# Optimization experiments

Measured on AMD Instinct MI355X. Metric: run time of the kernel, lower is better.

The kernel has to match this reference:

```python
import jax, jax.numpy as jnp
import numpy as np

N_NODES = 10000
IN_CH = 128
OUT_CH = 128
N_EDGES = 320000


def setup_inputs() -> dict:
    key = jax.random.key(0)
    k1, k2, k3, k4 = jax.random.split(key, 4)
    x = jax.random.normal(k1, (N_NODES, IN_CH), dtype=jnp.float32)
    edge_index = jax.random.randint(k2, (N_EDGES, 2), 0, N_NODES, dtype=jnp.int64)
    # Linear weights (torch stores [out, in]); scale like kaiming-uniform-ish
    w = jax.random.normal(k3, (OUT_CH, IN_CH), dtype=jnp.float32) / np.sqrt(IN_CH)
    b = jax.random.normal(k4, (OUT_CH, IN_CH), dtype=jnp.float32) / np.sqrt(IN_CH)
    return {"x": x, "edge_index": edge_index, "w": w, "b": b}


def reference(x, edge_index, w, b):
    n = x.shape[0]
    # Each edge (i, j) contributes x[j] to node i and x[i] to node j (undirected).
    src = jnp.concatenate([edge_index[:, 1], edge_index[:, 0]])  # feature source
    dst = jnp.concatenate([edge_index[:, 0], edge_index[:, 1]])  # aggregation target
    # segment-sum of gathered neighbor features -> [n, in_ch]
    agg_sum = jax.ops.segment_sum(x[src], dst, num_segments=n)
    deg = jax.ops.segment_sum(jnp.ones_like(dst, dtype=x.dtype), dst, num_segments=n)
    # mean with zero fallback for isolated nodes (original uses zeros vector)
    agg = jnp.where(deg[:, None] > 0, agg_sum / jnp.maximum(deg, 1.0)[:, None], 0.0)
    # out = ReLU(agg @ w^T + x @ b^T)
    return jax.nn.relu(agg @ w.T + x @ b.T)
```

## Files before the change

### kernel.cpp

```cpp
#include <hip/hip_runtime.h>

#define N_NODES 10000
#define CH 128
#define N_EDGES 320000
#define CAP 128
#define CSTR 16


__device__ __forceinline__ unsigned short f2bf(float f) {
    unsigned u = __float_as_uint(f);
    return (unsigned short)((u + 0x7FFFu + ((u >> 16) & 1u)) >> 16);
}
__device__ __forceinline__ float bf2f(unsigned short h) {
    return __uint_as_float(((unsigned)h) << 16);
}

__global__ __launch_bounds__(256) void fill_kernel(const int* __restrict__ ei,
                                                   int* __restrict__ cursor,
                                                   unsigned short* __restrict__ adj)
{
    const int t = blockIdx.x * blockDim.x + threadIdx.x;
    if (t >= N_EDGES) return;
    const int2 p = ((const int2*)ei)[t];
    if ((unsigned)p.x >= N_NODES || (unsigned)p.y >= N_NODES) return;
    const int s0 = atomicAdd(&cursor[p.x * CSTR], 1);
    const int s1 = atomicAdd(&cursor[p.y * CSTR], 1);
    if (s0 < CAP) adj[(size_t)p.x * CAP + s0] = (unsigned short)p.y;
    if (s1 < CAP) adj[(size_t)p.y * CAP + s1] = (unsigned short)p.x;
}

__global__ __launch_bounds__(256) void gather_kernel(const float* __restrict__ x,
                                                     const int* __restrict__ cursor,
                                                     const unsigned short* __restrict__ adj,
                                                     unsigned short* __restrict__ aggb)
{
    const int wv   = threadIdx.x >> 6;
    const int node = blockIdx.x * 4 + wv;
    const int lane = threadIdx.x & 63;
    const int h    = lane >> 5;
    const int l    = lane & 31;

    const int deg = cursor[node * CSTR];
    const int d   = deg < CAP ? deg : CAP;
    const unsigned short* nb = adj + (size_t)node * CAP;

    float4 acc = {0.f, 0.f, 0.f, 0.f};
    const int nit = (d + 1) >> 1;
#pragma unroll 4
    for (int it = 0; it < nit; ++it) {
        const int idx = 2 * it + h;
        int j = nb[idx];
        j = j < N_NODES ? j : 0;
        const float4 u = ((const float4*)(x + (size_t)j * CH))[l];
        const float m = idx < d ? 1.0f : 0.0f;
        acc.x += m * u.x; acc.y += m * u.y; acc.z += m * u.z; acc.w += m * u.w;
    }
    acc.x += __shfl_xor(acc.x, 32, 64);
    acc.y += __shfl_xor(acc.y, 32, 64);
    acc.z += __shfl_xor(acc.z, 32, 64);
    acc.w += __shfl_xor(acc.w, 32, 64);

    if (h == 0) {
        const float inv = deg > 0 ? 1.0f / (float)deg : 0.0f;
        ushort4 o;
        o.x = f2bf(acc.x * inv);
        o.y = f2bf(acc.y * inv);
        o.z = f2bf(acc.z * inv);
        o.w = f2bf(acc.w * inv);
        ((ushort4*)(aggb + (size_t)node * CH))[l] = o;
    }
}

#define NPB 16
__global__ __launch_bounds__(256) void gemm_relu_kernel(const unsigned short* __restrict__ aggb,
                                                        const float* __restrict__ x,
                                                        const float* __restrict__ w,
                                                        const float* __restrict__ b,
                                                        float* __restrict__ out)
{
    __shared__ float sh_a[NPB * CH];
    __shared__ float sh_x[NPB * CH];
    const int tid   = threadIdx.x;
    const int node0 = blockIdx.x * NPB;

    const ushort4* ag = (const ushort4*)(aggb + (size_t)node0 * CH);
#pragma unroll
    for (int r = 0; r < 2; ++r) {
        const ushort4 q = ag[tid + r * 256];
        const int base = (tid + r * 256) * 4;
        sh_a[base + 0] = bf2f(q.x);
        sh_a[base + 1] = bf2f(q.y);
        sh_a[base + 2] = bf2f(q.z);
        sh_a[base + 3] = bf2f(q.w);
    }
    ((float4*)sh_x)[tid]       = ((const float4*)(x + (size_t)node0 * CH))[tid];
    ((float4*)sh_x)[tid + 256] = ((const float4*)(x + (size_t)node0 * CH))[tid + 256];
    __syncthreads();

    const int o = tid & 127;
    const int g = tid >> 7;
    const float4* wr = (const float4*)(w + (size_t)o * CH);
    const float4* br = (const float4*)(b + (size_t)o * CH);
    const float4* A  = (const float4*)(sh_a + (size_t)(g * 8) * CH);
    const float4* X  = (const float4*)(sh_x + (size_t)(g * 8) * CH);

    float acc[8] = {0.f, 0.f, 0.f, 0.f, 0.f, 0.f, 0.f, 0.f};
#pragma unroll 4
    for (int k = 0; k < CH / 4; ++k) {
        const float4 wv = wr[k];
        const float4 bv = br[k];
#pragma unroll
        for (int n = 0; n < 8; ++n) {
            const float4 a4 = A[n * (CH / 4) + k];
            const float4 x4 = X[n * (CH / 4) + k];
            acc[n] += a4.x * wv.x + a4.y * wv.y + a4.z * wv.z + a4.w * wv.w
                    + x4.x * bv.x + x4.y * bv.y + x4.z * bv.z + x4.w * bv.w;
        }
    }
#pragma unroll
    for (int n = 0; n < 8; ++n) {
        const int node = node0 + g * 8 + n;
        const float v = acc[n];
        out[(size_t)node * CH + o] = v > 0.f ? v : 0.f;
    }
}

extern "C" void kernel_launch(void* const* d_in, const int* in_sizes, int n_in,
                              void* d_out, int out_size, void* d_ws, size_t ws_size,
                              hipStream_t stream)
{
    const float* x  = (const float*)d_in[0];
    const int*   ei = (const int*)d_in[1];
    const float* w  = (const float*)d_in[2];
    const float* b  = (const float*)d_in[3];
    float*       out = (float*)d_out;

    int*            cursor = (int*)d_ws;
    unsigned short* adj    = (unsigned short*)((char*)d_ws + 640000);
    unsigned short* aggb   = (unsigned short*)((char*)d_ws + 3200000);

    hipMemsetAsync(d_ws, 0, (size_t)N_NODES * CSTR * sizeof(int), stream);

    fill_kernel<<<(N_EDGES + 255) / 256, 256, 0, stream>>>(ei, cursor, adj);
    gather_kernel<<<N_NODES / 4, 256, 0, stream>>>(x, cursor, adj, aggb);
    gemm_relu_kernel<<<N_NODES / NPB, 256, 0, stream>>>(aggb, x, w, b, out);
}
```

Measured before the change: 140.4 us.

## Fuse gather into GEMM and gather from a bf16 copy of x

Adds a bf16 conversion of x to the edge-fill kernel, with each thread now handling two edges and converting eight floats. The gather is folded into the GEMM kernel: each block aggregates its 16 nodes straight into shared memory, so the aggregated intermediate is never written to or read back from global memory. Neighbour rows are read as bf16, halving gather traffic. The cost is fewer gather blocks (625 instead of 2500), which cuts the parallelism available to hide the random-access latency, and it adds bf16 rounding to the neighbour features.

```diff
diff --git a/kernel.cpp b/kernel.cpp
--- a/kernel.cpp
+++ b/kernel.cpp
@@ -5,6 +5,7 @@
 #define N_EDGES 320000
 #define CAP 128
 #define CSTR 16
+#define NPB 16
 
 
 __device__ __forceinline__ unsigned short f2bf(float f) {
@@ -15,86 +16,96 @@
     return __uint_as_float(((unsigned)h) << 16);
 }
 
-__global__ __launch_bounds__(256) void fill_kernel(const int* __restrict__ ei,
-                                                   int* __restrict__ cursor,
-                                                   unsigned short* __restrict__ adj)
+__global__ __launch_bounds__(256) void fill_convert_kernel(
+    const int* __restrict__ ei,
+    const float* __restrict__ x,
+    int* __restrict__ cursor,
+    unsigned short* __restrict__ adj,
+    unsigned short* __restrict__ xb)
 {
     const int t = blockIdx.x * blockDim.x + threadIdx.x;
-    if (t >= N_EDGES) return;
-    const int2 p = ((const int2*)ei)[t];
-    if ((unsigned)p.x >= N_NODES || (unsigned)p.y >= N_NODES) return;
-    const int s0 = atomicAdd(&cursor[p.x * CSTR], 1);
-    const int s1 = atomicAdd(&cursor[p.y * CSTR], 1);
-    if (s0 < CAP) adj[(size_t)p.x * CAP + s0] = (unsigned short)p.y;
-    if (s1 < CAP) adj[(size_t)p.y * CAP + s1] = (unsigned short)p.x;
-}
 
-__global__ __launch_bounds__(256) void gather_kernel(const float* __restrict__ x,
-                                                     const int* __restrict__ cursor,
-                                                     const unsigned short* __restrict__ adj,
-                                                     unsigned short* __restrict__ aggb)
-{
-    const int wv   = threadIdx.x >> 6;
-    const int node = blockIdx.x * 4 + wv;
-    const int lane = threadIdx.x & 63;
-    const int h    = lane >> 5;
-    const int l    = lane & 31;
+    const float4 c0 = ((const float4*)x)[2 * t];
+    const float4 c1 = ((const float4*)x)[2 * t + 1];
+    ushort4 o0, o1;
+    o0.x = f2bf(c0.x); o0.y = f2bf(c0.y); o0.z = f2bf(c0.z); o0.w = f2bf(c0.w);
+    o1.x = f2bf(c1.x); o1.y = f2bf(c1.y); o1.z = f2bf(c1.z); o1.w = f2bf(c1.w);
+    ((ushort4*)xb)[2 * t]     = o0;
+    ((ushort4*)xb)[2 * t + 1] = o1;
 
-    const int deg = cursor[node * CSTR];
-    const int d   = deg < CAP ? deg : CAP;
-    const unsigned short* nb = adj + (size_t)node * CAP;
-
-    float4 acc = {0.f, 0.f, 0.f, 0.f};
-    const int nit = (d + 1) >> 1;
-#pragma unroll 4
-    for (int it = 0; it < nit; ++it) {
-        const int idx = 2 * it + h;
-        int j = nb[idx];
-        j = j < N_NODES ? j : 0;
-        const float4 u = ((const float4*)(x + (size_t)j * CH))[l];
-        const float m = idx < d ? 1.0f : 0.0f;
-        acc.x += m * u.x; acc.y += m * u.y; acc.z += m * u.z; acc.w += m * u.w;
+    const int4 p = ((const int4*)ei)[t];
+    const bool v0 = (unsigned)p.x < N_NODES && (unsigned)p.y < N_NODES;
+    const bool v1 = (unsigned)p.z < N_NODES && (unsigned)p.w < N_NODES;
+    int s0 = 0, s1 = 0, s2 = 0, s3 = 0;
+    if (v0) { s0 = atomicAdd(&cursor[p.x * CSTR], 1); s1 = atomicAdd(&cursor[p.y * CSTR], 1); }
+    if (v1) { s2 = atomicAdd(&cursor[p.z * CSTR], 1); s3 = atomicAdd(&cursor[p.w * CSTR], 1); }
+    if (v0) {
+        if (s0 < CAP) adj[(size_t)p.x * CAP + s0] = (unsigned short)p.y;
+        if (s1 < CAP) adj[(size_t)p.y * CAP + s1] = (unsigned short)p.x;
     }
-    acc.x += __shfl_xor(acc.x, 32, 64);
-    acc.y += __shfl_xor(acc.y, 32, 64);
-    acc.z += __shfl_xor(acc.z, 32, 64);
-    acc.w += __shfl_xor(acc.w, 32, 64);
-
-    if (h == 0) {
-        const float inv = deg > 0 ? 1.0f / (float)deg : 0.0f;
-        ushort4 o;
-        o.x = f2bf(acc.x * inv);
-        o.y = f2bf(acc.y * inv);
-        o.z = f2bf(acc.z * inv);
-        o.w = f2bf(acc.w * inv);
-        ((ushort4*)(aggb + (size_t)node * CH))[l] = o;
+    if (v1) {
+        if (s2 < CAP) adj[(size_t)p.z * CAP + s2] = (unsigned short)p.w;
+        if (s3 < CAP) adj[(size_t)p.w * CAP + s3] = (unsigned short)p.z;
     }
 }
 
-#define NPB 16
-__global__ __launch_bounds__(256) void gemm_relu_kernel(const unsigned short* __restrict__ aggb,
-                                                        const float* __restrict__ x,
-                                                        const float* __restrict__ w,
-                                                        const float* __restrict__ b,
-                                                        float* __restrict__ out)
+__global__ __launch_bounds__(256) void gather_gemm_kernel(
+    const float* __restrict__ x,
+    const unsigned short* __restrict__ xb,
+    const int* __restrict__ cursor,
+    const unsigned short* __restrict__ adj,
+    const float* __restrict__ w,
+    const float* __restrict__ b,
+    float* __restrict__ out)
 {
     __shared__ float sh_a[NPB * CH];
     __shared__ float sh_x[NPB * CH];
     const int tid   = threadIdx.x;
     const int node0 = blockIdx.x * NPB;
 
-    const ushort4* ag = (const ushort4*)(aggb + (size_t)node0 * CH);
-#pragma unroll
-    for (int r = 0; r < 2; ++r) {
-        const ushort4 q = ag[tid + r * 256];
-        const int base = (tid + r * 256) * 4;
-        sh_a[base + 0] = bf2f(q.x);
-        sh_a[base + 1] = bf2f(q.y);
-        sh_a[base + 2] = bf2f(q.z);
-        sh_a[base + 3] = bf2f(q.w);
-    }
     ((float4*)sh_x)[tid]       = ((const float4*)(x + (size_t)node0 * CH))[tid];
     ((float4*)sh_x)[tid + 256] = ((const float4*)(x + (size_t)node0 * CH))[tid + 256];
+
+    {
+        const int wv   = tid >> 6;
+        const int lane = tid & 63;
+        const int h    = lane >> 5;
+        const int l    = lane & 31;
+#pragma unroll
+        for (int q = 0; q < 4; ++q) {
+            const int ln   = wv + 4 * q;
+            const int node = node0 + ln;
+            const int deg  = cursor[node * CSTR];
+            const int d    = deg < CAP ? deg : CAP;
+            const unsigned short* nb = adj + (size_t)node * CAP;
+
+            float4 acc = {0.f, 0.f, 0.f, 0.f};
+            const int nit = (d + 1) >> 1;
+#pragma unroll 4
+            for (int it = 0; it < nit; ++it) {
+                const int idx = 2 * it + h;
+                int j = nb[idx];
+                j = j < N_NODES ? j : 0;
+                const ushort4 u = ((const ushort4*)(xb + (size_t)j * CH))[l];
+                const float m = idx < d ? 1.0f : 0.0f;
+                acc.x += m * bf2f(u.x);
+                acc.y += m * bf2f(u.y);
+                acc.z += m * bf2f(u.z);
+                acc.w += m * bf2f(u.w);
+            }
+            acc.x += __shfl_xor(acc.x, 32, 64);
+            acc.y += __shfl_xor(acc.y, 32, 64);
+            acc.z += __shfl_xor(acc.z, 32, 64);
+            acc.w += __shfl_xor(acc.w, 32, 64);
+            if (h == 0) {
+                const float inv = deg > 0 ? 1.0f / (float)deg : 0.0f;
+                float4 o4;
+                o4.x = acc.x * inv; o4.y = acc.y * inv;
+                o4.z = acc.z * inv; o4.w = acc.w * inv;
+                ((float4*)(sh_a + (size_t)ln * CH))[l] = o4;
+            }
+        }
+    }
     __syncthreads();
 
     const int o = tid & 127;
@@ -107,14 +118,14 @@
     float acc[8] = {0.f, 0.f, 0.f, 0.f, 0.f, 0.f, 0.f, 0.f};
 #pragma unroll 4
     for (int k = 0; k < CH / 4; ++k) {
-        const float4 wv = wr[k];
-        const float4 bv = br[k];
+        const float4 wv4 = wr[k];
+        const float4 bv4 = br[k];
 #pragma unroll
         for (int n = 0; n < 8; ++n) {
             const float4 a4 = A[n * (CH / 4) + k];
             const float4 x4 = X[n * (CH / 4) + k];
-            acc[n] += a4.x * wv.x + a4.y * wv.y + a4.z * wv.z + a4.w * wv.w
-                    + x4.x * bv.x + x4.y * bv.y + x4.z * bv.z + x4.w * bv.w;
+            acc[n] += a4.x * wv4.x + a4.y * wv4.y + a4.z * wv4.z + a4.w * wv4.w
+                    + x4.x * bv4.x + x4.y * bv4.y + x4.z * bv4.z + x4.w * bv4.w;
         }
     }
 #pragma unroll
@@ -137,11 +148,10 @@
 
     int*            cursor = (int*)d_ws;
     unsigned short* adj    = (unsigned short*)((char*)d_ws + 640000);
-    unsigned short* aggb   = (unsigned short*)((char*)d_ws + 3200000);
+    unsigned short* xb     = (unsigned short*)((char*)d_ws + 3200000);
 
     hipMemsetAsync(d_ws, 0, (size_t)N_NODES * CSTR * sizeof(int), stream);
 
-    fill_kernel<<<(N_EDGES + 255) / 256, 256, 0, stream>>>(ei, cursor, adj);
-    gather_kernel<<<N_NODES / 4, 256, 0, stream>>>(x, cursor, adj, aggb);
-    gemm_relu_kernel<<<N_NODES / NPB, 256, 0, stream>>>(aggb, x, w, b, out);
+    fill_convert_kernel<<<625, 256, 0, stream>>>(ei, x, cursor, adj, xb);
+    gather_gemm_kernel<<<625, 256, 0, stream>>>(x, xb, cursor, adj, w, b, out);
 }
```

New measurement: 143.3 us. 2.0% more time.
